# Kernel optimization log

Hardware: AMD Instinct MI355X
Metric: run time of the kernel (lower is better)

## Reference

```python
import jax, jax.numpy as jnp
import numpy as np

B, C, H, W = 4, 64, 128, 128

def conv1x1(x, w, b):
    # x: [B,Ci,H,W], w: [Co,Ci], b: [Co]
    return jnp.einsum('bchw,oc->bohw', x, w) + b[None, :, None, None]

def setup_inputs() -> dict:
    key = jax.random.key(0)
    ks = jax.random.split(key, 10)
    d = {}
    d['x'] = jax.random.normal(ks[0], (B, C, H, W), dtype=jnp.float32)
    # patchmerging params: LayerNorm(4C) + Linear(4C -> C)
    d['pm_gamma'] = jnp.ones((4 * C,), jnp.float32)
    d['pm_beta'] = jnp.zeros((4 * C,), jnp.float32)
    d['pm_w'] = jax.random.normal(ks[1], (C, 4 * C), jnp.float32) * 0.02
    d['pm_b'] = jnp.zeros((C,), jnp.float32)
    # 1x1 convs: conv2..conv6 are C->C, conv1 is 2C->C
    for i, n in enumerate(['2', '3', '4', '5', '6']):
        d['w' + n] = jax.random.normal(ks[2 + i], (C, C), jnp.float32) * 0.05
        d['b' + n] = jnp.zeros((C,), jnp.float32)
    d['w1'] = jax.random.normal(ks[7], (C, 2 * C), jnp.float32) * 0.05
    d['b1'] = jnp.zeros((C,), jnp.float32)
    return d

def reference(x, pm_gamma, pm_beta, pm_w, pm_b,
              w1, b1, w2, b2, w3, b3, w4, b4, w5, b5, w6, b6):
    Bx, Cx, Hx, Wx = x.shape
    Hh, Wh = Hx // 2, Wx // 2
    N = Hh * Wh
    # ---- patch merging ----
    x0 = x[:, :, 0::2, 0::2]
    x1_ = x[:, :, 1::2, 0::2]
    x2_ = x[:, :, 0::2, 1::2]
    x3_ = x[:, :, 1::2, 1::2]
    m = jnp.concatenate([x0, x1_, x2_, x3_], axis=1)        # [B,4C,Hh,Wh]
    t = m.reshape(Bx, 4 * Cx, N).transpose(0, 2, 1)          # [B,N,4C]
    mu = t.mean(-1, keepdims=True)
    var = t.var(-1, keepdims=True)
    t = (t - mu) / jnp.sqrt(var + 1e-5) * pm_gamma + pm_beta  # LayerNorm eps=1e-5
    t = t @ pm_w.T + pm_b                                     # [B,N,C]
    c1 = t.transpose(0, 2, 1).reshape(Bx, Cx, Hh, Wh)
    # ---- spatial attention (PAM-style) ----
    q = conv1x1(c1, w2, b2).reshape(Bx, Cx, N)
    k = conv1x1(c1, w3, b3).reshape(Bx, Cx, N)
    v = conv1x1(c1, w4, b4).reshape(Bx, Cx, N)
    qk1 = jax.nn.softmax(jnp.einsum('bcn,bcm->bnm', q, k), axis=-1)  # [B,N,N]
    # torch: out1 = v @ qk1.permute(0,2,1) -> out1[b,c,j] = sum_i v[b,c,i]*qk1[b,j,i]
    out1 = jnp.einsum('bci,bji->bcj', v, qk1).reshape(Bx, Cx, Hh, Wh)
    # ---- channel attention (CAM-style) ----
    q2 = conv1x1(c1, w5, b5).reshape(Bx, Cx, N)
    k2 = conv1x1(c1, w6, b6).reshape(Bx, Cx, N)
    qk2 = jax.nn.softmax(jnp.einsum('bcn,bdn->bcd', q2, k2), axis=-1)  # [B,C,C]
    out2 = jnp.einsum('bcd,bdn->bcn', qk2, v).reshape(Bx, Cx, Hh, Wh)
    # ---- fuse, 1x1 conv, bilinear upsample x2 (align_corners=False), residual ----
    out = jnp.concatenate([out1, out2], axis=1)              # [B,2C,Hh,Wh]
    out = conv1x1(out, w1, b1)                               # [B,C,Hh,Wh]
    out = jax.image.resize(out, (Bx, Cx, Hx, Wx), method='bilinear')
    return out + x
```

## Files before the change

kernel.cpp:

```cpp
#include <hip/hip_runtime.h>

typedef __attribute__((ext_vector_type(8))) short bf16x8;
typedef __attribute__((ext_vector_type(4))) float fx4;

struct __attribute__((aligned(8))) sh4 { short x, y, z, w; };

#define OPART_B   0u
#define LSUM_B    12582912u
#define SMALL_B   12976128u
#define L2M_B     17170432u
#define C1B_B     17235968u
#define QB_B      19333120u
#define KB_B      21430272u
#define VCN_B     23527424u
#define VNC_B     25624576u
#define Q2B_B     27721728u
#define K2B_B     29818880u
#define PMB_B     31916032u
#define W2B_B     31948800u
#define W3B_B     31956992u
#define W4B_B     31965184u
#define W5B_B     31973376u
#define W6B_B     31981568u
#define W1B_B     31989760u

static __device__ __forceinline__ short f2bf(float f) {
  unsigned u = __float_as_uint(f);
  unsigned r = (u + 0x7FFFu + ((u >> 16) & 1u)) >> 16;
  return (short)r;
}
static __device__ __forceinline__ short f2bf_fast(float f) {
  return (short)((__float_as_uint(f) + 0x8000u) >> 16);
}
static __device__ __forceinline__ float bf2f(short s) {
  return __uint_as_float(((unsigned)(unsigned short)s) << 16);
}

__global__ __launch_bounds__(256) void prep_kernel(
    const float* __restrict__ pm_w, const float* __restrict__ w2,
    const float* __restrict__ w3,  const float* __restrict__ w4,
    const float* __restrict__ w5,  const float* __restrict__ w6,
    const float* __restrict__ w1,  char* __restrict__ wsb)
{
  int tid = blockIdx.x * 256 + threadIdx.x;
  ((short*)(wsb + PMB_B))[tid] = f2bf(pm_w[tid]);
  if (tid < 4096) {
    ((short*)(wsb + W2B_B))[tid] = f2bf(w2[tid]);
    ((short*)(wsb + W3B_B))[tid] = f2bf(w3[tid]);
    ((short*)(wsb + W4B_B))[tid] = f2bf(w4[tid]);
    ((short*)(wsb + W5B_B))[tid] = f2bf(w5[tid]);
    ((short*)(wsb + W6B_B))[tid] = f2bf(w6[tid]);
  }
  if (tid < 8192) ((short*)(wsb + W1B_B))[tid] = f2bf(w1[tid]);
  ((float*)(wsb + L2M_B))[tid] = 0.0f;
}

__global__ __launch_bounds__(256) void patchln_kernel(
    const float* __restrict__ x, const float* __restrict__ gamma,
    const float* __restrict__ beta, const short* __restrict__ pmb,
    const float* __restrict__ pm_b, short* __restrict__ c1b)
{
  __shared__ short tnb[32*264];
  __shared__ float red_s[512];
  __shared__ float mu_s[32], rs_s[32];
  const int b   = blockIdx.y;
  const int i   = blockIdx.x >> 1;
  const int jh  = blockIdx.x & 1;
  const int tid = threadIdx.x;
  const int j   = tid & 31;
  const int g8  = tid >> 5;
  const int jj  = jh*32 + j;

  float vals[32];
  float sm = 0.f, sq = 0.f;
  #pragma unroll
  for (int k = 0; k < 16; ++k) {
    int p  = g8*16 + k;
    int cc = p & 63, di = p >> 6;
    float2 v2 = *(const float2*)&x[((size_t)(b*64 + cc)*128 + 2*i + di)*128 + 2*jj];
    vals[2*k]   = v2.x;
    vals[2*k+1] = v2.y;
    sm += v2.x + v2.y; sq += v2.x*v2.x + v2.y*v2.y;
  }
  red_s[g8*32 + j] = sm;
  red_s[256 + g8*32 + j] = sq;
  __syncthreads();
  if (tid < 32) {
    float s0 = 0.f, q0 = 0.f;
    #pragma unroll
    for (int g = 0; g < 8; ++g) { s0 += red_s[g*32 + tid]; q0 += red_s[256 + g*32 + tid]; }
    float mu  = s0 * (1.0f/256.0f);
    float var = q0 * (1.0f/256.0f) - mu*mu;
    mu_s[tid] = mu;
    rs_s[tid] = rsqrtf(var + 1e-5f);
  }
  __syncthreads();
  {
    float mu = mu_s[j], rs = rs_s[j];
    #pragma unroll
    for (int k = 0; k < 16; ++k) {
      int p  = g8*16 + k;
      int ca = p, cb = p + 128;
      tnb[j*264 + ca] = f2bf((vals[2*k]   - mu)*rs*gamma[ca] + beta[ca]);
      tnb[j*264 + cb] = f2bf((vals[2*k+1] - mu)*rs*gamma[cb] + beta[cb]);
    }
  }
  __syncthreads();

  const int w    = tid >> 6;
  const int lane = tid & 63;
  const int L15  = lane & 15;
  const int quad = lane >> 4;
  fx4 d0 = {0.f,0.f,0.f,0.f}, d1 = {0.f,0.f,0.f,0.f};
  #pragma unroll
  for (int kc = 0; kc < 8; ++kc) {
    bf16x8 a  = *(const bf16x8*)&pmb[(w*16 + L15)*256 + kc*32 + quad*8];
    bf16x8 bf0 = *(const bf16x8*)&tnb[(L15)*264      + kc*32 + quad*8];
    bf16x8 bf1 = *(const bf16x8*)&tnb[(16 + L15)*264 + kc*32 + quad*8];
    d0 = __builtin_amdgcn_mfma_f32_16x16x32_bf16(a, bf0, d0, 0, 0, 0);
    d1 = __builtin_amdgcn_mfma_f32_16x16x32_bf16(a, bf1, d1, 0, 0, 0);
  }
  const int obase = w*16 + quad*4;
  float bias0 = pm_b[obase], bias1 = pm_b[obase+1], bias2 = pm_b[obase+2], bias3 = pm_b[obase+3];
  const int gn0 = i*64 + jh*32 + L15;
  sh4 s0; s0.x = f2bf(d0[0]+bias0); s0.y = f2bf(d0[1]+bias1); s0.z = f2bf(d0[2]+bias2); s0.w = f2bf(d0[3]+bias3);
  sh4 s1; s1.x = f2bf(d1[0]+bias0); s1.y = f2bf(d1[1]+bias1); s1.z = f2bf(d1[2]+bias2); s1.w = f2bf(d1[3]+bias3);
  *(sh4*)&c1b[((size_t)b*4096 + gn0)*64 + obase]      = s0;
  *(sh4*)&c1b[((size_t)b*4096 + gn0 + 16)*64 + obase] = s1;
}

__global__ __launch_bounds__(256) void proj5_kernel(
    const short* __restrict__ c1b,
    const short* __restrict__ w2b, const short* __restrict__ w3b, const short* __restrict__ w4b,
    const short* __restrict__ w5b, const short* __restrict__ w6b,
    const float* __restrict__ b2, const float* __restrict__ b3, const float* __restrict__ b4,
    const float* __restrict__ b5, const float* __restrict__ b6,
    short* __restrict__ qb, short* __restrict__ kb,
    short* __restrict__ vcn, short* __restrict__ vnc,
    short* __restrict__ q2b, short* __restrict__ k2b)
{
  __shared__ short ldsT[4*16*72];
  const int b    = blockIdx.y;
  const int tid  = threadIdx.x;
  const int w    = tid >> 6;
  const int nsub = w & 1;
  const int pg   = w >> 1;
  const int lane = tid & 63;
  const int L15  = lane & 15;
  const int quad = lane >> 4;
  const int gn0  = blockIdx.x*32 + nsub*16;
  const int gn   = gn0 + L15;
  short* T = ldsT + w*16*72;

  bf16x8 bf0 = *(const bf16x8*)&c1b[((size_t)b*4096 + gn)*64 + quad*8];
  bf16x8 bf1 = *(const bf16x8*)&c1b[((size_t)b*4096 + gn)*64 + quad*8 + 32];

  if (pg == 0) {
    const short* wp[2] = {w2b, w3b};
    const float* bp[2] = {b2, b3};
    #pragma unroll
    for (int p = 0; p < 2; ++p) {
      short* dst = (p == 0) ? qb : kb;
      #pragma unroll
      for (int mt = 0; mt < 4; ++mt) {
        bf16x8 a0 = *(const bf16x8*)&wp[p][(mt*16 + L15)*64 + quad*8];
        bf16x8 a1 = *(const bf16x8*)&wp[p][(mt*16 + L15)*64 + quad*8 + 32];
        fx4 d = {0.f,0.f,0.f,0.f};
        d = __builtin_amdgcn_mfma_f32_16x16x32_bf16(a0, bf0, d, 0, 0, 0);
        d = __builtin_amdgcn_mfma_f32_16x16x32_bf16(a1, bf1, d, 0, 0, 0);
        const int ob = mt*16 + quad*4;
        sh4 s; s.x = f2bf(d[0]+bp[p][ob]); s.y = f2bf(d[1]+bp[p][ob+1]);
        s.z = f2bf(d[2]+bp[p][ob+2]); s.w = f2bf(d[3]+bp[p][ob+3]);
        *(sh4*)&dst[((size_t)b*4096 + gn)*64 + ob] = s;
      }
    }
    #pragma unroll
    for (int mt = 0; mt < 4; ++mt) {
      bf16x8 a0 = *(const bf16x8*)&w4b[(mt*16 + L15)*64 + quad*8];
      bf16x8 a1 = *(const bf16x8*)&w4b[(mt*16 + L15)*64 + quad*8 + 32];
      fx4 d = {0.f,0.f,0.f,0.f};
      d = __builtin_amdgcn_mfma_f32_16x16x32_bf16(a0, bf0, d, 0, 0, 0);
      d = __builtin_amdgcn_mfma_f32_16x16x32_bf16(a1, bf1, d, 0, 0, 0);
      const int ob = mt*16 + quad*4;
      sh4 s; s.x = f2bf(d[0]+b4[ob]); s.y = f2bf(d[1]+b4[ob+1]);
      s.z = f2bf(d[2]+b4[ob+2]); s.w = f2bf(d[3]+b4[ob+3]);
      *(sh4*)&vnc[((size_t)b*4096 + gn)*64 + ob] = s;
      *(sh4*)&T[L15*72 + ob] = s;
    }
    {
      const int o = lane;
      bf16x8 r0, r1;
      #pragma unroll
      for (int n = 0; n < 8; ++n) r0[n] = T[n*72 + o];
      #pragma unroll
      for (int n = 0; n < 8; ++n) r1[n] = T[(n+8)*72 + o];
      *(bf16x8*)&vcn[(size_t)b*262144 + (size_t)o*4096 + gn0]     = r0;
      *(bf16x8*)&vcn[(size_t)b*262144 + (size_t)o*4096 + gn0 + 8] = r1;
    }
  } else {
    const short* wp[2] = {w5b, w6b};
    const float* bp[2] = {b5, b6};
    #pragma unroll
    for (int p = 0; p < 2; ++p) {
      short* dst = (p == 0) ? q2b : k2b;
      #pragma unroll
      for (int mt = 0; mt < 4; ++mt) {
        bf16x8 a0 = *(const bf16x8*)&wp[p][(mt*16 + L15)*64 + quad*8];
        bf16x8 a1 = *(const bf16x8*)&wp[p][(mt*16 + L15)*64 + quad*8 + 32];
        fx4 d = {0.f,0.f,0.f,0.f};
        d = __builtin_amdgcn_mfma_f32_16x16x32_bf16(a0, bf0, d, 0, 0, 0);
        d = __builtin_amdgcn_mfma_f32_16x16x32_bf16(a1, bf1, d, 0, 0, 0);
        const int ob = mt*16 + quad*4;
        sh4 s; s.x = f2bf(d[0]+bp[p][ob]); s.y = f2bf(d[1]+bp[p][ob+1]);
        s.z = f2bf(d[2]+bp[p][ob+2]); s.w = f2bf(d[3]+bp[p][ob+3]);
        *(sh4*)&T[L15*72 + ob] = s;
      }
      const int o = lane;
      bf16x8 r0, r1;
      #pragma unroll
      for (int n = 0; n < 8; ++n) r0[n] = T[n*72 + o];
      #pragma unroll
      for (int n = 0; n < 8; ++n) r1[n] = T[(n+8)*72 + o];
      *(bf16x8*)&dst[(size_t)b*262144 + (size_t)o*4096 + gn0]     = r0;
      *(bf16x8*)&dst[(size_t)b*262144 + (size_t)o*4096 + gn0 + 8] = r1;
    }
  }
}

__global__ __launch_bounds__(256) void flash_kernel(
    const short* __restrict__ Qb, const short* __restrict__ Kb,
    const short* __restrict__ Vcn, short* __restrict__ opart, float* __restrict__ lsum)
{
  __shared__ short lds_s[24576];
  short* ktb = lds_s;
  short* vsb = lds_s + 8192;
  short* ps  = lds_s + 16384;

  const int b    = blockIdx.z;
  const int s    = blockIdx.y;
  const int q0   = blockIdx.x << 7;
  const int t0   = (s < 4) ? s*11 : 44 + (s - 4)*10;
  const int cnt  = (s < 4) ? 11 : 10;
  const int tid  = threadIdx.x;
  const int w    = tid >> 6;
  const int lane = tid & 63;
  const int L15  = lane & 15;
  const int quad = lane >> 4;
  const int jbase = w*32;

  const short* Qg = Qb  + (size_t)b*262144;
  const short* Kg = Kb  + (size_t)b*262144;
  const short* Vg = Vcn + (size_t)b*262144;

  bf16x8 qa[2][2];
  #pragma unroll
  for (int jt = 0; jt < 2; ++jt)
    #pragma unroll
    for (int h = 0; h < 2; ++h)
      qa[jt][h] = *(const bf16x8*)(Qg + (size_t)(q0 + jbase + jt*16 + L15)*64 + h*32 + quad*8);

  bf16x8 ones;
  #pragma unroll
  for (int u = 0; u < 8; ++u) ones[u] = (short)0x3F80;

  const int si  = tid >> 2;
  const int scb = (tid & 3) * 2;
  const int s0k = scb ^ (si & 7);
  const int s1k = s0k ^ 1;

  {
    const int i0 = t0 << 6;
    bf16x8 kr0 = *(const bf16x8*)(Kg + (size_t)(i0 + si)*64 + scb*8);
    bf16x8 kr1 = *(const bf16x8*)(Kg + (size_t)(i0 + si)*64 + scb*8 + 8);
    bf16x8 vr0 = *(const bf16x8*)(Vg + (size_t)si*4096 + i0 + (tid&3)*16);
    bf16x8 vr1 = *(const bf16x8*)(Vg + (size_t)si*4096 + i0 + (tid&3)*16 + 8);
    *(bf16x8*)(ktb + si*64 + s0k*8) = kr0;
    *(bf16x8*)(ktb + si*64 + s1k*8) = kr1;
    *(bf16x8*)(vsb + si*64 + s0k*8) = vr0;
    *(bf16x8*)(vsb + si*64 + s1k*8) = vr1;
  }
  __syncthreads();

  fx4 oacc[2][4];
  #pragma unroll
  for (int jt = 0; jt < 2; ++jt)
    #pragma unroll
    for (int ct = 0; ct < 4; ++ct) oacc[jt][ct] = (fx4){0.f,0.f,0.f,0.f};
  fx4 lacc[2] = {{0.f,0.f,0.f,0.f},{0.f,0.f,0.f,0.f}};

  const int cbx0 = quad       ^ (L15 & 7);
  const int cbx1 = (quad + 4) ^ (L15 & 7);
  const int jk   = L15 & 7;
  const int pu   = (quad >> 1);
  const int ph   = (quad & 1) << 2;

  for (int t = 0; t < cnt; ++t) {
    const short* kt = ktb + (t & 1)*4096;
    const short* vv = vsb + (t & 1)*4096;
    short* ktn = ktb + ((t + 1) & 1)*4096;
    short* vsn = vsb + ((t + 1) & 1)*4096;

    bf16x8 kr0, kr1, vr0, vr1;
    const bool pf = (t < cnt - 1);
    if (pf) {
      const int i0n = (t0 + t + 1) << 6;
      kr0 = *(const bf16x8*)(Kg + (size_t)(i0n + si)*64 + scb*8);
      kr1 = *(const bf16x8*)(Kg + (size_t)(i0n + si)*64 + scb*8 + 8);
      vr0 = *(const bf16x8*)(Vg + (size_t)si*4096 + i0n + (tid&3)*16);
      vr1 = *(const bf16x8*)(Vg + (size_t)si*4096 + i0n + (tid&3)*16 + 8);
    }

    fx4 d2[4][2];
    #pragma unroll
    for (int mt = 0; mt < 4; ++mt)
      #pragma unroll
      for (int jt = 0; jt < 2; ++jt) d2[mt][jt] = (fx4){0.f,0.f,0.f,0.f};
    #pragma unroll
    for (int mt = 0; mt < 4; ++mt) {
      bf16x8 ak0 = *(const bf16x8*)(kt + (mt*16 + L15)*64 + cbx0*8);
      bf16x8 ak1 = *(const bf16x8*)(kt + (mt*16 + L15)*64 + cbx1*8);
      d2[mt][0] = __builtin_amdgcn_mfma_f32_16x16x32_bf16(ak0, qa[0][0], d2[mt][0], 0, 0, 0);
      d2[mt][1] = __builtin_amdgcn_mfma_f32_16x16x32_bf16(ak0, qa[1][0], d2[mt][1], 0, 0, 0);
      d2[mt][0] = __builtin_amdgcn_mfma_f32_16x16x32_bf16(ak1, qa[0][1], d2[mt][0], 0, 0, 0);
      d2[mt][1] = __builtin_amdgcn_mfma_f32_16x16x32_bf16(ak1, qa[1][1], d2[mt][1], 0, 0, 0);
    }

    #pragma unroll
    for (int mt = 0; mt < 4; ++mt) {
      const int slot0 = ((mt*2 + pu) ^ jk) << 3;
      #pragma unroll
      for (int jt = 0; jt < 2; ++jt) {
        const int j = jbase + jt*16 + L15;
        sh4 pv;
        pv.x = f2bf_fast(__expf(d2[mt][jt][0]));
        pv.y = f2bf_fast(__expf(d2[mt][jt][1]));
        pv.z = f2bf_fast(__expf(d2[mt][jt][2]));
        pv.w = f2bf_fast(__expf(d2[mt][jt][3]));
        *(sh4*)&ps[j*64 + slot0 + ph] = pv;
      }
    }

    bf16x8 pb[2][2];
    #pragma unroll
    for (int jt = 0; jt < 2; ++jt) {
      const int jrow = jbase + jt*16 + L15;
      pb[jt][0] = *(const bf16x8*)&ps[jrow*64 + (((quad    ) ^ jk) << 3)];
      pb[jt][1] = *(const bf16x8*)&ps[jrow*64 + (((quad + 4) ^ jk) << 3)];
    }

    #pragma unroll
    for (int jt = 0; jt < 2; ++jt) {
      lacc[jt] = __builtin_amdgcn_mfma_f32_16x16x32_bf16(ones, pb[jt][0], lacc[jt], 0, 0, 0);
      lacc[jt] = __builtin_amdgcn_mfma_f32_16x16x32_bf16(ones, pb[jt][1], lacc[jt], 0, 0, 0);
    }

    #pragma unroll
    for (int ct = 0; ct < 4; ++ct) {
      bf16x8 va0 = *(const bf16x8*)(vv + (ct*16 + L15)*64 + cbx0*8);
      bf16x8 va1 = *(const bf16x8*)(vv + (ct*16 + L15)*64 + cbx1*8);
      #pragma unroll
      for (int jt = 0; jt < 2; ++jt) {
        oacc[jt][ct] = __builtin_amdgcn_mfma_f32_16x16x32_bf16(va0, pb[jt][0], oacc[jt][ct], 0, 0, 0);
        oacc[jt][ct] = __builtin_amdgcn_mfma_f32_16x16x32_bf16(va1, pb[jt][1], oacc[jt][ct], 0, 0, 0);
      }
    }

    if (pf) {
      *(bf16x8*)(ktn + si*64 + s0k*8) = kr0;
      *(bf16x8*)(ktn + si*64 + s1k*8) = kr1;
      *(bf16x8*)(vsn + si*64 + s0k*8) = vr0;
      *(bf16x8*)(vsn + si*64 + s1k*8) = vr1;
    }
    __syncthreads();
  }

  const size_t srow = ((size_t)(b*6 + s)*4096) + q0;
  #pragma unroll
  for (int jt = 0; jt < 2; ++jt) {
    const size_t nrow = srow + jbase + jt*16 + L15;
    #pragma unroll
    for (int ct = 0; ct < 4; ++ct) {
      sh4 sv;
      sv.x = f2bf(oacc[jt][ct][0]); sv.y = f2bf(oacc[jt][ct][1]);
      sv.z = f2bf(oacc[jt][ct][2]); sv.w = f2bf(oacc[jt][ct][3]);
      *(sh4*)&opart[nrow*64 + ct*16 + quad*4] = sv;
    }
    if (quad == 0) lsum[nrow] = lacc[jt][0];
  }
}

__global__ __launch_bounds__(256) void corr_kernel(
    const short* __restrict__ q2b, const short* __restrict__ k2b, float* __restrict__ L2M)
{
  const int b    = blockIdx.y;
  const int n0   = blockIdx.x * 128;
  const int tid  = threadIdx.x;
  const int w    = tid >> 6;
  const int lane = tid & 63;
  const int L15  = lane & 15;
  const int quad = lane >> 4;
  const short* qg = q2b + (size_t)b*262144;
  const short* kg = k2b + (size_t)b*262144;
  fx4 D[4] = {{0.f,0.f,0.f,0.f},{0.f,0.f,0.f,0.f},{0.f,0.f,0.f,0.f},{0.f,0.f,0.f,0.f}};
  #pragma unroll
  for (int kc = 0; kc < 4; ++kc) {
    bf16x8 a = *(const bf16x8*)&qg[(w*16 + L15)*4096 + n0 + kc*32 + quad*8];
    #pragma unroll
    for (int nt = 0; nt < 4; ++nt) {
      bf16x8 bb = *(const bf16x8*)&kg[(nt*16 + L15)*4096 + n0 + kc*32 + quad*8];
      D[nt] = __builtin_amdgcn_mfma_f32_16x16x32_bf16(a, bb, D[nt], 0, 0, 0);
    }
  }
  float* Lb = L2M + (size_t)b*4096;
  #pragma unroll
  for (int nt = 0; nt < 4; ++nt)
    #pragma unroll
    for (int r = 0; r < 4; ++r)
      atomicAdd(&Lb[(w*16 + quad*4 + r)*64 + nt*16 + L15], D[nt][r]);
}

__global__ __launch_bounds__(256) void tail_kernel(
    const short* __restrict__ opart, const float* __restrict__ lsum,
    const float* __restrict__ l2m, const short* __restrict__ vnc,
    const short* __restrict__ w1b, const float* __restrict__ b1,
    float* __restrict__ sml)
{
  __shared__ short p2[4096];
  __shared__ short cat[8192];
  const int b    = blockIdx.y;
  const int n0   = blockIdx.x << 6;
  const int tid  = threadIdx.x;
  const int w    = tid >> 6;
  const int lane = tid & 63;
  const int L15  = lane & 15;
  const int quad = lane >> 4;

  if (tid < 64) {
    const float* Lr = l2m + (size_t)b*4096 + tid*64;
    float vrow[64];
    float mx = -1e30f;
    #pragma unroll
    for (int d4 = 0; d4 < 16; ++d4) {
      float4 v4 = *(const float4*)&Lr[d4*4];
      vrow[d4*4+0] = v4.x; vrow[d4*4+1] = v4.y; vrow[d4*4+2] = v4.z; vrow[d4*4+3] = v4.w;
      mx = fmaxf(mx, fmaxf(fmaxf(v4.x, v4.y), fmaxf(v4.z, v4.w)));
    }
    float sme = 0.f;
    #pragma unroll
    for (int d = 0; d < 64; ++d) { vrow[d] = __expf(vrow[d] - mx); sme += vrow[d]; }
    const float inv = 1.0f / sme;
    const int key = tid & 7;
    #pragma unroll
    for (int g = 0; g < 8; ++g) {
      bf16x8 pk;
      #pragma unroll
      for (int u = 0; u < 8; ++u) pk[u] = f2bf(vrow[g*8 + u] * inv);
      *(bf16x8*)&p2[tid*64 + ((g ^ key) << 3)] = pk;
    }
  }

  {
    const int nl = tid >> 2;
    const int c0 = (tid & 3) << 4;
    const int n  = n0 + nl;
    float l = 0.f;
    #pragma unroll
    for (int sp = 0; sp < 6; ++sp) l += lsum[((size_t)(b*6 + sp)*4096) + n];
    const float inv = 1.0f / l;
    float acc[16];
    #pragma unroll
    for (int u = 0; u < 16; ++u) acc[u] = 0.f;
    #pragma unroll
    for (int sp = 0; sp < 6; ++sp) {
      const short* pp = opart + (((size_t)(b*6 + sp)*4096) + n)*64 + c0;
      bf16x8 A0 = *(const bf16x8*)pp;
      bf16x8 A1 = *(const bf16x8*)(pp + 8);
      #pragma unroll
      for (int u = 0; u < 8; ++u) { acc[u] += bf2f(A0[u]); acc[8+u] += bf2f(A1[u]); }
    }
    const int key = nl & 7;
    #pragma unroll
    for (int gi = 0; gi < 2; ++gi) {
      const int g = ((c0 >> 3) + gi) ^ key;
      sh4 s0, s1;
      s0.x = f2bf(acc[gi*8+0]*inv); s0.y = f2bf(acc[gi*8+1]*inv);
      s0.z = f2bf(acc[gi*8+2]*inv); s0.w = f2bf(acc[gi*8+3]*inv);
      s1.x = f2bf(acc[gi*8+4]*inv); s1.y = f2bf(acc[gi*8+5]*inv);
      s1.z = f2bf(acc[gi*8+6]*inv); s1.w = f2bf(acc[gi*8+7]*inv);
      *(sh4*)&cat[nl*128 + g*8]     = s0;
      *(sh4*)&cat[nl*128 + g*8 + 4] = s1;
    }
  }
  __syncthreads();

  {
    const int nl  = w*16 + L15;
    const int n   = n0 + nl;
    const int key = L15 & 7;
    bf16x8 vb0 = *(const bf16x8*)&vnc[((size_t)b*4096 + n)*64 + quad*8];
    bf16x8 vb1 = *(const bf16x8*)&vnc[((size_t)b*4096 + n)*64 + quad*8 + 32];
    #pragma unroll
    for (int mt = 0; mt < 4; ++mt) {
      bf16x8 a0 = *(const bf16x8*)&p2[(mt*16 + L15)*64 + (((quad    ) ^ key) << 3)];
      bf16x8 a1 = *(const bf16x8*)&p2[(mt*16 + L15)*64 + (((quad + 4) ^ key) << 3)];
      fx4 d = {0.f,0.f,0.f,0.f};
      d = __builtin_amdgcn_mfma_f32_16x16x32_bf16(a0, vb0, d, 0, 0, 0);
      d = __builtin_amdgcn_mfma_f32_16x16x32_bf16(a1, vb1, d, 0, 0, 0);
      const int c = 64 + mt*16 + quad*4;
      const int g = (c >> 3) ^ key;
      sh4 sv; sv.x = f2bf(d[0]); sv.y = f2bf(d[1]); sv.z = f2bf(d[2]); sv.w = f2bf(d[3]);
      *(sh4*)&cat[nl*128 + g*8 + (quad & 1)*4] = sv;
    }
  }
  __syncthreads();

  {
    const int nl  = w*16 + L15;
    const int key = L15 & 7;
    bf16x8 bfr[4];
    #pragma unroll
    for (int kc = 0; kc < 4; ++kc) {
      const int g = (kc*4 + quad) ^ key;
      bfr[kc] = *(const bf16x8*)&cat[nl*128 + g*8];
    }
    #pragma unroll
    for (int mt = 0; mt < 4; ++mt) {
      fx4 d = {0.f,0.f,0.f,0.f};
      #pragma unroll
      for (int kc = 0; kc < 4; ++kc) {
        bf16x8 a = *(const bf16x8*)&w1b[(mt*16 + L15)*128 + kc*32 + quad*8];
        d = __builtin_amdgcn_mfma_f32_16x16x32_bf16(a, bfr[kc], d, 0, 0, 0);
      }
      const int ob = mt*16 + quad*4;
      #pragma unroll
      for (int r = 0; r < 4; ++r)
        sml[((size_t)b*64 + ob + r)*4096 + n0 + nl] = d[r] + b1[ob + r];
    }
  }
}

__global__ __launch_bounds__(256) void upsample_kernel(
    const float* __restrict__ sml, const float* __restrict__ x, float* __restrict__ out)
{
  int idx = blockIdx.x*256 + threadIdx.x;
  int jp = idx & 63;
  int I  = (idx >> 6) & 127;
  int bo = idx >> 13;
  int ih = I >> 1;
  int i0, i1; float wi0, wi1;
  if (I & 1) { i0 = ih;                 i1 = (ih < 63) ? ih+1 : 63; wi0 = 0.75f; wi1 = 0.25f; }
  else       { i0 = (ih > 0) ? ih-1 : 0; i1 = ih;                   wi0 = 0.25f; wi1 = 0.75f; }
  const int jm = (jp > 0)  ? jp-1 : 0;
  const int jx = (jp < 63) ? jp+1 : 63;
  const float* sp = sml + (size_t)bo*4096;
  float a0 = sp[i0*64 + jm], a1 = sp[i0*64 + jp], a2 = sp[i0*64 + jx];
  float b0 = sp[i1*64 + jm], b1v = sp[i1*64 + jp], b2v = sp[i1*64 + jx];
  float re0 = wi0*(0.25f*a0 + 0.75f*a1) + wi1*(0.25f*b0 + 0.75f*b1v);
  float re1 = wi0*(0.75f*a1 + 0.25f*a2) + wi1*(0.75f*b1v + 0.25f*b2v);
  const size_t obase = ((size_t)bo*128 + I)*128 + jp*2;
  float2 xr = *(const float2*)&x[obase];
  *(float2*)&out[obase] = make_float2(re0 + xr.x, re1 + xr.y);
}

extern "C" void kernel_launch(void* const* d_in, const int* in_sizes, int n_in,
                              void* d_out, int out_size, void* d_ws, size_t ws_size,
                              hipStream_t stream) {
  const float* x     = (const float*)d_in[0];
  const float* gamma = (const float*)d_in[1];
  const float* beta  = (const float*)d_in[2];
  const float* pm_w  = (const float*)d_in[3];
  const float* pm_b  = (const float*)d_in[4];
  const float* w2 = (const float*)d_in[5];  const float* b2 = (const float*)d_in[6];
  const float* w3 = (const float*)d_in[7];  const float* b3 = (const float*)d_in[8];
  const float* w4 = (const float*)d_in[9];  const float* b4 = (const float*)d_in[10];
  const float* w5 = (const float*)d_in[11]; const float* b5 = (const float*)d_in[12];
  const float* w6 = (const float*)d_in[13]; const float* b6 = (const float*)d_in[14];
  const float* w1 = (const float*)d_in[15]; const float* b1 = (const float*)d_in[16];
  char* wsb  = (char*)d_ws;
  float* out = (float*)d_out;

  short* opart = (short*)(wsb + OPART_B);
  float* lsum  = (float*)(wsb + LSUM_B);
  float* sml   = (float*)(wsb + SMALL_B);
  float* l2m   = (float*)(wsb + L2M_B);
  short* c1b   = (short*)(wsb + C1B_B);
  short* qb    = (short*)(wsb + QB_B);
  short* kb    = (short*)(wsb + KB_B);
  short* vcn   = (short*)(wsb + VCN_B);
  short* vnc   = (short*)(wsb + VNC_B);
  short* q2b   = (short*)(wsb + Q2B_B);
  short* k2b   = (short*)(wsb + K2B_B);
  short* pmb   = (short*)(wsb + PMB_B);
  short* w2b   = (short*)(wsb + W2B_B);
  short* w3b   = (short*)(wsb + W3B_B);
  short* w4b   = (short*)(wsb + W4B_B);
  short* w5b   = (short*)(wsb + W5B_B);
  short* w6b   = (short*)(wsb + W6B_B);
  short* w1b   = (short*)(wsb + W1B_B);

  prep_kernel<<<dim3(64), dim3(256), 0, stream>>>(pm_w, w2, w3, w4, w5, w6, w1, wsb);
  patchln_kernel<<<dim3(128,4), dim3(256), 0, stream>>>(x, gamma, beta, pmb, pm_b, c1b);
  proj5_kernel<<<dim3(128,4), dim3(256), 0, stream>>>(c1b, w2b, w3b, w4b, w5b, w6b,
      b2, b3, b4, b5, b6, qb, kb, vcn, vnc, q2b, k2b);
  flash_kernel<<<dim3(32,6,4), dim3(256), 0, stream>>>(qb, kb, vcn, opart, lsum);
  corr_kernel<<<dim3(32,4), dim3(256), 0, stream>>>(q2b, k2b, l2m);
  tail_kernel<<<dim3(64,4), dim3(256), 0, stream>>>(opart, lsum, l2m, vnc, w1b, b1, sml);
  upsample_kernel<<<dim3(8192), dim3(256), 0, stream>>>(sml, x, out);
}
```

Measured before the change: 161.7 us.

## Remove prep and corr launches; convert weights inline, fold corr into flash grid

```diff
diff --git a/kernel.cpp b/kernel.cpp
--- a/kernel.cpp
+++ b/kernel.cpp
@@ -16,13 +16,6 @@
 #define VNC_B     25624576u
 #define Q2B_B     27721728u
 #define K2B_B     29818880u
-#define PMB_B     31916032u
-#define W2B_B     31948800u
-#define W3B_B     31956992u
-#define W4B_B     31965184u
-#define W5B_B     31973376u
-#define W6B_B     31981568u
-#define W1B_B     31989760u
 
 static __device__ __forceinline__ short f2bf(float f) {
   unsigned u = __float_as_uint(f);
@@ -35,30 +28,19 @@
 static __device__ __forceinline__ float bf2f(short s) {
   return __uint_as_float(((unsigned)(unsigned short)s) << 16);
 }
-
-__global__ __launch_bounds__(256) void prep_kernel(
-    const float* __restrict__ pm_w, const float* __restrict__ w2,
-    const float* __restrict__ w3,  const float* __restrict__ w4,
-    const float* __restrict__ w5,  const float* __restrict__ w6,
-    const float* __restrict__ w1,  char* __restrict__ wsb)
-{
-  int tid = blockIdx.x * 256 + threadIdx.x;
-  ((short*)(wsb + PMB_B))[tid] = f2bf(pm_w[tid]);
-  if (tid < 4096) {
-    ((short*)(wsb + W2B_B))[tid] = f2bf(w2[tid]);
-    ((short*)(wsb + W3B_B))[tid] = f2bf(w3[tid]);
-    ((short*)(wsb + W4B_B))[tid] = f2bf(w4[tid]);
-    ((short*)(wsb + W5B_B))[tid] = f2bf(w5[tid]);
-    ((short*)(wsb + W6B_B))[tid] = f2bf(w6[tid]);
-  }
-  if (tid < 8192) ((short*)(wsb + W1B_B))[tid] = f2bf(w1[tid]);
-  ((float*)(wsb + L2M_B))[tid] = 0.0f;
+static __device__ __forceinline__ bf16x8 ld8f(const float* p) {
+  float4 p0 = *(const float4*)p;
+  float4 p1 = *(const float4*)(p + 4);
+  bf16x8 r;
+  r[0] = f2bf(p0.x); r[1] = f2bf(p0.y); r[2] = f2bf(p0.z); r[3] = f2bf(p0.w);
+  r[4] = f2bf(p1.x); r[5] = f2bf(p1.y); r[6] = f2bf(p1.z); r[7] = f2bf(p1.w);
+  return r;
 }
 
 __global__ __launch_bounds__(256) void patchln_kernel(
     const float* __restrict__ x, const float* __restrict__ gamma,
-    const float* __restrict__ beta, const short* __restrict__ pmb,
-    const float* __restrict__ pm_b, short* __restrict__ c1b)
+    const float* __restrict__ beta, const float* __restrict__ pm_w,
+    const float* __restrict__ pm_b, short* __restrict__ c1b, float* __restrict__ l2m)
 {
   __shared__ short tnb[32*264];
   __shared__ float red_s[512];
@@ -71,6 +53,11 @@
   const int g8  = tid >> 5;
   const int jj  = jh*32 + j;
 
+  if (blockIdx.x == 0) {
+    #pragma unroll
+    for (int k = 0; k < 16; ++k) l2m[(size_t)b*4096 + k*256 + tid] = 0.0f;
+  }
+
   float vals[32];
   float sm = 0.f, sq = 0.f;
   #pragma unroll
@@ -114,7 +101,7 @@
   fx4 d0 = {0.f,0.f,0.f,0.f}, d1 = {0.f,0.f,0.f,0.f};
   #pragma unroll
   for (int kc = 0; kc < 8; ++kc) {
-    bf16x8 a  = *(const bf16x8*)&pmb[(w*16 + L15)*256 + kc*32 + quad*8];
+    bf16x8 a = ld8f(pm_w + (w*16 + L15)*256 + kc*32 + quad*8);
     bf16x8 bf0 = *(const bf16x8*)&tnb[(L15)*264      + kc*32 + quad*8];
     bf16x8 bf1 = *(const bf16x8*)&tnb[(16 + L15)*264 + kc*32 + quad*8];
     d0 = __builtin_amdgcn_mfma_f32_16x16x32_bf16(a, bf0, d0, 0, 0, 0);
@@ -131,8 +118,8 @@
 
 __global__ __launch_bounds__(256) void proj5_kernel(
     const short* __restrict__ c1b,
-    const short* __restrict__ w2b, const short* __restrict__ w3b, const short* __restrict__ w4b,
-    const short* __restrict__ w5b, const short* __restrict__ w6b,
+    const float* __restrict__ w2f, const float* __restrict__ w3f, const float* __restrict__ w4f,
+    const float* __restrict__ w5f, const float* __restrict__ w6f,
     const float* __restrict__ b2, const float* __restrict__ b3, const float* __restrict__ b4,
     const float* __restrict__ b5, const float* __restrict__ b6,
     short* __restrict__ qb, short* __restrict__ kb,
@@ -156,15 +143,15 @@
   bf16x8 bf1 = *(const bf16x8*)&c1b[((size_t)b*4096 + gn)*64 + quad*8 + 32];
 
   if (pg == 0) {
-    const short* wp[2] = {w2b, w3b};
+    const float* wp[2] = {w2f, w3f};
     const float* bp[2] = {b2, b3};
     #pragma unroll
     for (int p = 0; p < 2; ++p) {
       short* dst = (p == 0) ? qb : kb;
       #pragma unroll
       for (int mt = 0; mt < 4; ++mt) {
-        bf16x8 a0 = *(const bf16x8*)&wp[p][(mt*16 + L15)*64 + quad*8];
-        bf16x8 a1 = *(const bf16x8*)&wp[p][(mt*16 + L15)*64 + quad*8 + 32];
+        bf16x8 a0 = ld8f(wp[p] + (mt*16 + L15)*64 + quad*8);
+        bf16x8 a1 = ld8f(wp[p] + (mt*16 + L15)*64 + quad*8 + 32);
         fx4 d = {0.f,0.f,0.f,0.f};
         d = __builtin_amdgcn_mfma_f32_16x16x32_bf16(a0, bf0, d, 0, 0, 0);
         d = __builtin_amdgcn_mfma_f32_16x16x32_bf16(a1, bf1, d, 0, 0, 0);
@@ -176,8 +163,8 @@
     }
     #pragma unroll
     for (int mt = 0; mt < 4; ++mt) {
-      bf16x8 a0 = *(const bf16x8*)&w4b[(mt*16 + L15)*64 + quad*8];
-      bf16x8 a1 = *(const bf16x8*)&w4b[(mt*16 + L15)*64 + quad*8 + 32];
+      bf16x8 a0 = ld8f(w4f + (mt*16 + L15)*64 + quad*8);
+      bf16x8 a1 = ld8f(w4f + (mt*16 + L15)*64 + quad*8 + 32);
       fx4 d = {0.f,0.f,0.f,0.f};
       d = __builtin_amdgcn_mfma_f32_16x16x32_bf16(a0, bf0, d, 0, 0, 0);
       d = __builtin_amdgcn_mfma_f32_16x16x32_bf16(a1, bf1, d, 0, 0, 0);
@@ -198,15 +185,15 @@
       *(bf16x8*)&vcn[(size_t)b*262144 + (size_t)o*4096 + gn0 + 8] = r1;
     }
   } else {
-    const short* wp[2] = {w5b, w6b};
+    const float* wp[2] = {w5f, w6f};
     const float* bp[2] = {b5, b6};
     #pragma unroll
     for (int p = 0; p < 2; ++p) {
       short* dst = (p == 0) ? q2b : k2b;
       #pragma unroll
       for (int mt = 0; mt < 4; ++mt) {
-        bf16x8 a0 = *(const bf16x8*)&wp[p][(mt*16 + L15)*64 + quad*8];
-        bf16x8 a1 = *(const bf16x8*)&wp[p][(mt*16 + L15)*64 + quad*8 + 32];
+        bf16x8 a0 = ld8f(wp[p] + (mt*16 + L15)*64 + quad*8);
+        bf16x8 a1 = ld8f(wp[p] + (mt*16 + L15)*64 + quad*8 + 32);
         fx4 d = {0.f,0.f,0.f,0.f};
         d = __builtin_amdgcn_mfma_f32_16x16x32_bf16(a0, bf0, d, 0, 0, 0);
         d = __builtin_amdgcn_mfma_f32_16x16x32_bf16(a1, bf1, d, 0, 0, 0);
@@ -229,23 +216,48 @@
 
 __global__ __launch_bounds__(256) void flash_kernel(
     const short* __restrict__ Qb, const short* __restrict__ Kb,
-    const short* __restrict__ Vcn, short* __restrict__ opart, float* __restrict__ lsum)
+    const short* __restrict__ Vcn, short* __restrict__ opart, float* __restrict__ lsum,
+    const short* __restrict__ q2b, const short* __restrict__ k2b, float* __restrict__ L2M)
 {
   __shared__ short lds_s[24576];
-  short* ktb = lds_s;
-  short* vsb = lds_s + 8192;
-  short* ps  = lds_s + 16384;
-
   const int b    = blockIdx.z;
   const int s    = blockIdx.y;
-  const int q0   = blockIdx.x << 7;
-  const int t0   = (s < 4) ? s*11 : 44 + (s - 4)*10;
-  const int cnt  = (s < 4) ? 11 : 10;
   const int tid  = threadIdx.x;
   const int w    = tid >> 6;
   const int lane = tid & 63;
   const int L15  = lane & 15;
   const int quad = lane >> 4;
+
+  if (s == 6) {
+    const int n0 = blockIdx.x * 128;
+    const short* qg = q2b + (size_t)b*262144;
+    const short* kg = k2b + (size_t)b*262144;
+    fx4 D[4] = {{0.f,0.f,0.f,0.f},{0.f,0.f,0.f,0.f},{0.f,0.f,0.f,0.f},{0.f,0.f,0.f,0.f}};
+    #pragma unroll
+    for (int kc = 0; kc < 4; ++kc) {
+      bf16x8 a = *(const bf16x8*)&qg[(w*16 + L15)*4096 + n0 + kc*32 + quad*8];
+      #pragma unroll
+      for (int nt = 0; nt < 4; ++nt) {
+        bf16x8 bb = *(const bf16x8*)&kg[(nt*16 + L15)*4096 + n0 + kc*32 + quad*8];
+        D[nt] = __builtin_amdgcn_mfma_f32_16x16x32_bf16(a, bb, D[nt], 0, 0, 0);
+      }
+    }
+    float* Lb = L2M + (size_t)b*4096;
+    #pragma unroll
+    for (int nt = 0; nt < 4; ++nt)
+      #pragma unroll
+      for (int r = 0; r < 4; ++r)
+        atomicAdd(&Lb[(w*16 + quad*4 + r)*64 + nt*16 + L15], D[nt][r]);
+    return;
+  }
+
+  short* ktb = lds_s;
+  short* vsb = lds_s + 8192;
+  short* ps  = lds_s + 16384;
+
+  const int q0   = blockIdx.x << 7;
+  const int t0   = (s < 4) ? s*11 : 44 + (s - 4)*10;
+  const int cnt  = (s < 4) ? 11 : 10;
   const int jbase = w*32;
 
   const short* Qg = Qb  + (size_t)b*262144;
@@ -389,51 +401,21 @@
   }
 }
 
-__global__ __launch_bounds__(256) void corr_kernel(
-    const short* __restrict__ q2b, const short* __restrict__ k2b, float* __restrict__ L2M)
+__global__ __launch_bounds__(256) void tail_kernel(
+    const short* __restrict__ opart, const float* __restrict__ lsum,
+    const float* __restrict__ l2m, const short* __restrict__ vnc,
+    const float* __restrict__ w1f, const float* __restrict__ b1,
+    float* __restrict__ sml)
 {
+  __shared__ short p2[4096];
+  __shared__ short cat[4096];
   const int b    = blockIdx.y;
-  const int n0   = blockIdx.x * 128;
+  const int n0   = blockIdx.x << 5;
   const int tid  = threadIdx.x;
   const int w    = tid >> 6;
   const int lane = tid & 63;
   const int L15  = lane & 15;
   const int quad = lane >> 4;
-  const short* qg = q2b + (size_t)b*262144;
-  const short* kg = k2b + (size_t)b*262144;
-  fx4 D[4] = {{0.f,0.f,0.f,0.f},{0.f,0.f,0.f,0.f},{0.f,0.f,0.f,0.f},{0.f,0.f,0.f,0.f}};
-  #pragma unroll
-  for (int kc = 0; kc < 4; ++kc) {
-    bf16x8 a = *(const bf16x8*)&qg[(w*16 + L15)*4096 + n0 + kc*32 + quad*8];
-    #pragma unroll
-    for (int nt = 0; nt < 4; ++nt) {
-      bf16x8 bb = *(const bf16x8*)&kg[(nt*16 + L15)*4096 + n0 + kc*32 + quad*8];
-      D[nt] = __builtin_amdgcn_mfma_f32_16x16x32_bf16(a, bb, D[nt], 0, 0, 0);
-    }
-  }
-  float* Lb = L2M + (size_t)b*4096;
-  #pragma unroll
-  for (int nt = 0; nt < 4; ++nt)
-    #pragma unroll
-    for (int r = 0; r < 4; ++r)
-      atomicAdd(&Lb[(w*16 + quad*4 + r)*64 + nt*16 + L15], D[nt][r]);
-}
-
-__global__ __launch_bounds__(256) void tail_kernel(
-    const short* __restrict__ opart, const float* __restrict__ lsum,
-    const float* __restrict__ l2m, const short* __restrict__ vnc,
-    const short* __restrict__ w1b, const float* __restrict__ b1,
-    float* __restrict__ sml)
-{
-  __shared__ short p2[4096];
-  __shared__ short cat[8192];
-  const int b    = blockIdx.y;
-  const int n0   = blockIdx.x << 6;
-  const int tid  = threadIdx.x;
-  const int w    = tid >> 6;
-  const int lane = tid & 63;
-  const int L15  = lane & 15;
-  const int quad = lane >> 4;
 
   if (tid < 64) {
     const float* Lr = l2m + (size_t)b*4096 + tid*64;
@@ -460,47 +442,41 @@
   }
 
   {
-    const int nl = tid >> 2;
-    const int c0 = (tid & 3) << 4;
+    const int nl = tid >> 3;
+    const int c0 = (tid & 7) << 3;
     const int n  = n0 + nl;
     float l = 0.f;
     #pragma unroll
     for (int sp = 0; sp < 6; ++sp) l += lsum[((size_t)(b*6 + sp)*4096) + n];
     const float inv = 1.0f / l;
-    float acc[16];
-    #pragma unroll
-    for (int u = 0; u < 16; ++u) acc[u] = 0.f;
+    float acc[8];
+    #pragma unroll
+    for (int u = 0; u < 8; ++u) acc[u] = 0.f;
     #pragma unroll
     for (int sp = 0; sp < 6; ++sp) {
-      const short* pp = opart + (((size_t)(b*6 + sp)*4096) + n)*64 + c0;
-      bf16x8 A0 = *(const bf16x8*)pp;
-      bf16x8 A1 = *(const bf16x8*)(pp + 8);
-      #pragma unroll
-      for (int u = 0; u < 8; ++u) { acc[u] += bf2f(A0[u]); acc[8+u] += bf2f(A1[u]); }
+      bf16x8 A0 = *(const bf16x8*)&opart[(((size_t)(b*6 + sp)*4096) + n)*64 + c0];
+      #pragma unroll
+      for (int u = 0; u < 8; ++u) acc[u] += bf2f(A0[u]);
     }
     const int key = nl & 7;
-    #pragma unroll
-    for (int gi = 0; gi < 2; ++gi) {
-      const int g = ((c0 >> 3) + gi) ^ key;
-      sh4 s0, s1;
-      s0.x = f2bf(acc[gi*8+0]*inv); s0.y = f2bf(acc[gi*8+1]*inv);
-      s0.z = f2bf(acc[gi*8+2]*inv); s0.w = f2bf(acc[gi*8+3]*inv);
-      s1.x = f2bf(acc[gi*8+4]*inv); s1.y = f2bf(acc[gi*8+5]*inv);
-      s1.z = f2bf(acc[gi*8+6]*inv); s1.w = f2bf(acc[gi*8+7]*inv);
-      *(sh4*)&cat[nl*128 + g*8]     = s0;
-      *(sh4*)&cat[nl*128 + g*8 + 4] = s1;
-    }
+    const int g = (c0 >> 3) ^ key;
+    bf16x8 s0;
+    #pragma unroll
+    for (int u = 0; u < 8; ++u) s0[u] = f2bf(acc[u]*inv);
+    *(bf16x8*)&cat[nl*128 + (g << 3)] = s0;
   }
   __syncthreads();
 
   {
-    const int nl  = w*16 + L15;
+    const int nl  = (w & 1)*16 + L15;
     const int n   = n0 + nl;
+    const int mh  = w >> 1;
     const int key = L15 & 7;
     bf16x8 vb0 = *(const bf16x8*)&vnc[((size_t)b*4096 + n)*64 + quad*8];
     bf16x8 vb1 = *(const bf16x8*)&vnc[((size_t)b*4096 + n)*64 + quad*8 + 32];
     #pragma unroll
-    for (int mt = 0; mt < 4; ++mt) {
+    for (int mi = 0; mi < 2; ++mi) {
+      const int mt = mh*2 + mi;
       bf16x8 a0 = *(const bf16x8*)&p2[(mt*16 + L15)*64 + (((quad    ) ^ key) << 3)];
       bf16x8 a1 = *(const bf16x8*)&p2[(mt*16 + L15)*64 + (((quad + 4) ^ key) << 3)];
       fx4 d = {0.f,0.f,0.f,0.f};
@@ -509,26 +485,28 @@
       const int c = 64 + mt*16 + quad*4;
       const int g = (c >> 3) ^ key;
       sh4 sv; sv.x = f2bf(d[0]); sv.y = f2bf(d[1]); sv.z = f2bf(d[2]); sv.w = f2bf(d[3]);
-      *(sh4*)&cat[nl*128 + g*8 + (quad & 1)*4] = sv;
+      *(sh4*)&cat[nl*128 + (g << 3) + (quad & 1)*4] = sv;
     }
   }
   __syncthreads();
 
   {
-    const int nl  = w*16 + L15;
+    const int nl  = (w & 1)*16 + L15;
+    const int mh  = w >> 1;
     const int key = L15 & 7;
     bf16x8 bfr[4];
     #pragma unroll
     for (int kc = 0; kc < 4; ++kc) {
       const int g = (kc*4 + quad) ^ key;
-      bfr[kc] = *(const bf16x8*)&cat[nl*128 + g*8];
-    }
-    #pragma unroll
-    for (int mt = 0; mt < 4; ++mt) {
+      bfr[kc] = *(const bf16x8*)&cat[nl*128 + (g << 3)];
+    }
+    #pragma unroll
+    for (int mi = 0; mi < 2; ++mi) {
+      const int mt = mh*2 + mi;
       fx4 d = {0.f,0.f,0.f,0.f};
       #pragma unroll
       for (int kc = 0; kc < 4; ++kc) {
-        bf16x8 a = *(const bf16x8*)&w1b[(mt*16 + L15)*128 + kc*32 + quad*8];
+        bf16x8 a = ld8f(w1f + (mt*16 + L15)*128 + kc*32 + quad*8);
         d = __builtin_amdgcn_mfma_f32_16x16x32_bf16(a, bfr[kc], d, 0, 0, 0);
       }
       const int ob = mt*16 + quad*4;
@@ -590,20 +568,11 @@
   short* vnc   = (short*)(wsb + VNC_B);
   short* q2b   = (short*)(wsb + Q2B_B);
   short* k2b   = (short*)(wsb + K2B_B);
-  short* pmb   = (short*)(wsb + PMB_B);
-  short* w2b   = (short*)(wsb + W2B_B);
-  short* w3b   = (short*)(wsb + W3B_B);
-  short* w4b   = (short*)(wsb + W4B_B);
-  short* w5b   = (short*)(wsb + W5B_B);
-  short* w6b   = (short*)(wsb + W6B_B);
-  short* w1b   = (short*)(wsb + W1B_B);
-
-  prep_kernel<<<dim3(64), dim3(256), 0, stream>>>(pm_w, w2, w3, w4, w5, w6, w1, wsb);
-  patchln_kernel<<<dim3(128,4), dim3(256), 0, stream>>>(x, gamma, beta, pmb, pm_b, c1b);
-  proj5_kernel<<<dim3(128,4), dim3(256), 0, stream>>>(c1b, w2b, w3b, w4b, w5b, w6b,
+
+  patchln_kernel<<<dim3(128,4), dim3(256), 0, stream>>>(x, gamma, beta, pm_w, pm_b, c1b, l2m);
+  proj5_kernel<<<dim3(128,4), dim3(256), 0, stream>>>(c1b, w2, w3, w4, w5, w6,
       b2, b3, b4, b5, b6, qb, kb, vcn, vnc, q2b, k2b);
-  flash_kernel<<<dim3(32,6,4), dim3(256), 0, stream>>>(qb, kb, vcn, opart, lsum);
-  corr_kernel<<<dim3(32,4), dim3(256), 0, stream>>>(q2b, k2b, l2m);
-  tail_kernel<<<dim3(64,4), dim3(256), 0, stream>>>(opart, lsum, l2m, vnc, w1b, b1, sml);
+  flash_kernel<<<dim3(32,7,4), dim3(256), 0, stream>>>(qb, kb, vcn, opart, lsum, q2b, k2b, l2m);
+  tail_kernel<<<dim3(128,4), dim3(256), 0, stream>>>(opart, lsum, l2m, vnc, w1, b1, sml);
   upsample_kernel<<<dim3(8192), dim3(256), 0, stream>>>(sml, x, out);
 }
```

Result: no change. 163.1 us (+0.9%).
